# Kernel optimization log

Measured on AMD Instinct MI355X. Metric: run time of the kernel, lower is better.

Reference implementation:

```python
import jax, jax.numpy as jnp
import numpy as np

B, C, H, W = 64, 128, 32, 32
GROUPS = 32
EPS = 1e-6
SCALE = 0.044194173824159216  # 1/sqrt(512), as hardcoded in the torch module


def setup_inputs() -> dict:
    key = jax.random.key(0)
    ks = jax.random.split(key, 12)
    s = 1.0 / np.sqrt(C)
    return {
        "x": jax.random.normal(ks[0], (B, C, H, W), dtype=jnp.float32),
        "gn_w": jax.random.normal(ks[1], (C,), dtype=jnp.float32) * 0.02 + 1.0,
        "gn_b": jax.random.normal(ks[2], (C,), dtype=jnp.float32) * 0.02,
        "wq": jax.random.uniform(ks[3], (C, C), jnp.float32, -s, s),
        "bq": jax.random.uniform(ks[4], (C,), jnp.float32, -s, s),
        "wk": jax.random.uniform(ks[5], (C, C), jnp.float32, -s, s),
        "bk": jax.random.uniform(ks[6], (C,), jnp.float32, -s, s),
        "wv": jax.random.uniform(ks[7], (C, C), jnp.float32, -s, s),
        "bv": jax.random.uniform(ks[8], (C,), jnp.float32, -s, s),
        "wo": jax.random.uniform(ks[9], (C, C), jnp.float32, -s, s),
        "bo": jax.random.uniform(ks[10], (C,), jnp.float32, -s, s),
    }


def reference(x, gn_w, gn_b, wq, bq, wk, bk, wv, bv, wo, bo):
    b = x.shape[0]
    res = x
    # GroupNorm(32 groups, 128 channels): normalize over (channels_per_group, H, W)
    xg = x.reshape(b, GROUPS, C // GROUPS, H * W)
    mean = xg.mean(axis=(2, 3), keepdims=True)
    var = xg.var(axis=(2, 3), keepdims=True)
    xn = (xg - mean) * jax.lax.rsqrt(var + EPS)
    xn = xn.reshape(b, C, H, W) * gn_w[:, None, None] + gn_b[:, None, None]
    # flatten spatial -> sequence: [b, S=1024, C=128]
    t = xn.reshape(b, C, H * W).transpose(0, 2, 1)
    q = t @ wq.T + bq
    k = t @ wk.T + bk
    v = t @ wv.T + bv
    att = jnp.einsum('bsc,btc->bst', q, k) * SCALE  # [b, S, S]
    att = jax.nn.softmax(att, axis=-1)
    o = jnp.einsum('bst,btc->bsc', att, v)
    o = o @ wo.T + bo
    out = o.transpose(0, 2, 1).reshape(b, C, H, W) + res
    return out
```

## Files before the change

kernel.cpp:

```cpp
#include <hip/hip_runtime.h>
#include <hip/hip_bf16.h>

#define BATCH 64
#define CCH 128
#define SEQ 1024
#define NG 32
#define EPSV 1e-6f
#define SCALEV 0.044194173824159216f

typedef short v8s __attribute__((ext_vector_type(8)));
typedef short v4s __attribute__((ext_vector_type(4)));
typedef float v4f __attribute__((ext_vector_type(4)));
typedef int   v4i __attribute__((ext_vector_type(4)));
typedef unsigned short us;

__device__ __forceinline__ us f2bf(float f) {
    __hip_bfloat16 h = __float2bfloat16(f);
    return *reinterpret_cast<us*>(&h);
}

#define MFMA16(a, b, c) __builtin_amdgcn_mfma_f32_16x16x32_bf16(a, b, c, 0, 0, 0)

__device__ __forceinline__ void gld_lds16(const us* g, us* l) {
    __builtin_amdgcn_global_load_lds(
        (const __attribute__((address_space(1))) void*)g,
        (__attribute__((address_space(3))) void*)l, 16, 0, 0);
}

__global__ void prep_gn(const float* __restrict__ wq, const float* __restrict__ wk,
                        const float* __restrict__ wv, const float* __restrict__ wo,
                        us* wbf, const float* __restrict__ x,
                        float* meanr, float* rstdr) {
    int tid = threadIdx.x;
    if (blockIdx.x < 256) {
        int i = blockIdx.x * 256 + tid;
        const float* srcs[4] = {wq, wk, wv, wo};
        wbf[i] = f2bf(srcs[i >> 14][i & 16383]);
        return;
    }
    int bg = blockIdx.x - 256;
    const float4* p = (const float4*)(x + (size_t)bg * (4 * SEQ));
    float s1 = 0.f, s2 = 0.f;
    #pragma unroll
    for (int i = 0; i < 4; i++) {
        float4 v = p[i * 256 + tid];
        s1 += v.x + v.y + v.z + v.w;
        s2 += v.x * v.x + v.y * v.y + v.z * v.z + v.w * v.w;
    }
    #pragma unroll
    for (int off = 32; off; off >>= 1) {
        s1 += __shfl_down(s1, off);
        s2 += __shfl_down(s2, off);
    }
    __shared__ float a1[4], a2[4];
    int w = tid >> 6, l = tid & 63;
    if (l == 0) { a1[w] = s1; a2[w] = s2; }
    __syncthreads();
    if (tid == 0) {
        float t1 = a1[0] + a1[1] + a1[2] + a1[3];
        float t2 = a2[0] + a2[1] + a2[2] + a2[3];
        float mean = t1 * (1.0f / (4 * SEQ));
        float var  = t2 * (1.0f / (4 * SEQ)) - mean * mean;
        meanr[bg] = mean;
        rstdr[bg] = rsqrtf(var + EPSV);
    }
}

__global__ __launch_bounds__(256, 2) void qkv_kernel(
    const float* __restrict__ x, const float* __restrict__ gn_w,
    const float* __restrict__ gn_b, const float* __restrict__ meanr,
    const float* __restrict__ rstdr, const us* __restrict__ wbf,
    const float* __restrict__ bq, const float* __restrict__ bk,
    const float* __restrict__ bv,
    us* Q, us* K, us* Vt)
{
    __shared__ us tls[64 * 136];
    int b  = blockIdx.x >> 4;
    int s0 = (blockIdx.x & 15) * 64;
    int tid = threadIdx.x;
    const float* xb = x + (size_t)b * CCH * SEQ;

    for (int rep = 0; rep < 32; rep++) {
        int idx = rep * 256 + tid;
        int c = idx >> 6, s = idx & 63;
        float v = xb[c * SEQ + s0 + s];
        int g = c >> 2;
        float t = (v - meanr[b * NG + g]) * rstdr[b * NG + g] * gn_w[c] + gn_b[c];
        tls[s * 136 + c] = f2bf(t);
    }
    __syncthreads();

    int w = tid >> 6, lane = tid & 63;
    int m = lane & 15, quad = lane >> 4;

    v8s bfr[6][4];
    float bias[6];
    #pragma unroll
    for (int t = 0; t < 6; t++) {
        int T = w * 6 + t;
        int o = T >> 3, ct = T & 7;
        const us* wmat = wbf + o * 16384;
        #pragma unroll
        for (int ch = 0; ch < 4; ch++)
            bfr[t][ch] = *(const v8s*)&wmat[(ct * 16 + m) * 128 + ch * 32 + quad * 8];
        const float* bb = (o == 0) ? bq : (o == 1) ? bk : bv;
        bias[t] = bb[ct * 16 + m];
    }

    us* Qb = Q + (size_t)b * SEQ * CCH;
    us* Kb = K + (size_t)b * SEQ * CCH;
    us* Vb = Vt + (size_t)b * CCH * SEQ;

    #pragma unroll
    for (int st = 0; st < 4; st++) {
        v8s a[4];
        #pragma unroll
        for (int ch = 0; ch < 4; ch++)
            a[ch] = *(const v8s*)&tls[(st * 16 + m) * 136 + ch * 32 + quad * 8];
        int srow = s0 + st * 16 + quad * 4;
        #pragma unroll
        for (int t = 0; t < 6; t++) {
            int T = w * 6 + t;
            int o = T >> 3, ct = T & 7;
            v4f acc = {0,0,0,0};
            #pragma unroll
            for (int ch = 0; ch < 4; ch++)
                acc = MFMA16(a[ch], bfr[t][ch], acc);
            int col = ct * 16 + m;
            if (o < 2) {
                us* dst = (o == 0) ? Qb : Kb;
                #pragma unroll
                for (int r = 0; r < 4; r++)
                    dst[(size_t)(srow + r) * 128 + col] = f2bf(acc[r] + bias[t]);
            } else {
                v4s pk;
                #pragma unroll
                for (int r = 0; r < 4; r++) pk[r] = (short)f2bf(acc[r] + bias[t]);
                *(v4s*)&Vb[(size_t)col * SEQ + srow] = pk;
            }
        }
    }
}

__global__ __launch_bounds__(128, 2) void attn_kernel(
    const us* __restrict__ Q, const us* __restrict__ K,
    const us* __restrict__ Vt, const us* __restrict__ wbo,
    const float* __restrict__ bo, const float* __restrict__ x,
    float* __restrict__ out)
{
    __shared__ char smem_raw[32768];
    us* klds = (us*)smem_raw;
    us* vlds = (us*)(smem_raw + 16384);
    us* olds = (us*)smem_raw;

    int i = blockIdx.x;
    int b  = (i & 7) * 8 + ((i >> 3) & 7);
    int qt = i >> 6;
    int tid = threadIdx.x;
    int w = tid >> 6, lane = tid & 63;
    int m = lane & 15, quad = lane >> 4;
    int qrow0 = qt * 64 + w * 32;
    const us* Qb = Q + (size_t)b * SEQ * CCH;
    const us* Kb = K + (size_t)b * SEQ * CCH;
    const us* Vb = Vt + (size_t)b * CCH * SEQ;

    v8s aq[2][4];
    #pragma unroll
    for (int st = 0; st < 2; st++)
        #pragma unroll
        for (int ch = 0; ch < 4; ch++)
            aq[st][ch] = *(const v8s*)&Qb[(size_t)(qrow0 + st * 16 + m) * 128 + ch * 32 + quad * 8];

    v4f oacc[2][8];
    #pragma unroll
    for (int st = 0; st < 2; st++)
        #pragma unroll
        for (int ct = 0; ct < 8; ct++) oacc[st][ct] = (v4f){0, 0, 0, 0};
    float lrun[2] = {0.f, 0.f};

    const us* kg[8]; const us* vg[8];
    #pragma unroll
    for (int j8 = 0; j8 < 8; j8++) {
        int j = w * 8 + j8;
        int kr = 4 * j + (lane >> 4);
        kg[j8] = Kb + (size_t)kr * 128 + ((lane & 15) ^ (kr & 15)) * 8;
        int vc = 8 * j + (lane >> 3);
        vg[j8] = Vb + (size_t)vc * SEQ + ((lane & 7) ^ (vc & 7)) * 8;
    }
    int idx0 = 2 * (quad & 1) * 16 + m;
    int idx1 = idx0 + 16;

    for (int kt = 0; kt < 16; kt++) {
        __syncthreads();
        #pragma unroll
        for (int j8 = 0; j8 < 8; j8++) {
            int j = w * 8 + j8;
            gld_lds16(kg[j8] + kt * 8192, klds + j * 512);
            gld_lds16(vg[j8] + kt * 64,   vlds + j * 512);
        }
        __syncthreads();

        int e[2][4][2];
        #pragma unroll
        for (int c2 = 0; c2 < 4; c2++) {
            int krow = c2 * 16 + m;
            v4f acc0 = {0,0,0,0}, acc1 = {0,0,0,0};
            #pragma unroll
            for (int ch = 0; ch < 4; ch++) {
                int chunk = (ch * 4 + quad) ^ (krow & 15);
                v8s kb = *(const v8s*)&klds[krow * 128 + chunk * 8];
                acc0 = MFMA16(kb, aq[0][ch], acc0);
                acc1 = MFMA16(kb, aq[1][ch], acc1);
            }
            float p0[4], p1[4];
            #pragma unroll
            for (int r = 0; r < 4; r++) {
                p0[r] = __expf(acc0[r] * SCALEV);
                p1[r] = __expf(acc1[r] * SCALEV);
                lrun[0] += p0[r];
                lrun[1] += p1[r];
            }
            e[0][c2][0] = (int)f2bf(p0[0]) | ((int)f2bf(p0[1]) << 16);
            e[0][c2][1] = (int)f2bf(p0[2]) | ((int)f2bf(p0[3]) << 16);
            e[1][c2][0] = (int)f2bf(p1[0]) | ((int)f2bf(p1[1]) << 16);
            e[1][c2][1] = (int)f2bf(p1[2]) | ((int)f2bf(p1[3]) << 16);
        }
        v8s pa[2][2];
        #pragma unroll
        for (int st = 0; st < 2; st++)
            #pragma unroll
            for (int kc2 = 0; kc2 < 2; kc2++) {
                int c0 = (quad < 2) ? e[st][2 * kc2][0] : e[st][2 * kc2 + 1][0];
                int c1 = (quad < 2) ? e[st][2 * kc2][1] : e[st][2 * kc2 + 1][1];
                v4i t;
                t[0] = __shfl(c0, idx0);
                t[1] = __shfl(c1, idx0);
                t[2] = __shfl(c0, idx1);
                t[3] = __shfl(c1, idx1);
                pa[st][kc2] = __builtin_bit_cast(v8s, t);
            }
        #pragma unroll
        for (int ct = 0; ct < 8; ct++) {
            int vrow = ct * 16 + m;
            #pragma unroll
            for (int kc2 = 0; kc2 < 2; kc2++) {
                int chunk = (kc2 * 4 + quad) ^ (vrow & 7);
                v8s vb = *(const v8s*)&vlds[vrow * 64 + chunk * 8];
                oacc[0][ct] = MFMA16(pa[0][kc2], vb, oacc[0][ct]);
                oacc[1][ct] = MFMA16(pa[1][kc2], vb, oacc[1][ct]);
            }
        }
    }
    float inv[2][4];
    #pragma unroll
    for (int st = 0; st < 2; st++) {
        float rs = lrun[st];
        rs += __shfl_xor(rs, 16);
        rs += __shfl_xor(rs, 32);
        #pragma unroll
        for (int r = 0; r < 4; r++)
            inv[st][r] = 1.0f / __shfl(rs, quad * 4 + r);
    }
    __syncthreads();
    #pragma unroll
    for (int st = 0; st < 2; st++)
        #pragma unroll
        for (int ct = 0; ct < 8; ct++)
            #pragma unroll
            for (int r = 0; r < 4; r++)
                olds[(w * 32 + st * 16 + quad * 4 + r) * 136 + ct * 16 + m] =
                    f2bf(oacc[st][ct][r] * inv[st][r]);
    __syncthreads();
    const float* xb = x + (size_t)b * CCH * SEQ;
    float* ob = out + (size_t)b * CCH * SEQ;
    int sbase = qt * 64 + w * 32;
    v8s obf[2][4];
    #pragma unroll
    for (int st = 0; st < 2; st++)
        #pragma unroll
        for (int ch = 0; ch < 4; ch++)
            obf[st][ch] = *(const v8s*)&olds[(w * 32 + st * 16 + m) * 136 + ch * 32 + quad * 8];
    #pragma unroll
    for (int mt = 0; mt < 8; mt++) {
        v8s af[4];
        #pragma unroll
        for (int ch = 0; ch < 4; ch++)
            af[ch] = *(const v8s*)&wbo[(mt * 16 + m) * 128 + ch * 32 + quad * 8];
        #pragma unroll
        for (int st = 0; st < 2; st++) {
            v4f acc = {0,0,0,0};
            #pragma unroll
            for (int ch = 0; ch < 4; ch++)
                acc = MFMA16(af[ch], obf[st][ch], acc);
            #pragma unroll
            for (int r = 0; r < 4; r++) {
                int c = mt * 16 + quad * 4 + r;
                int idx = c * SEQ + sbase + st * 16 + m;
                ob[idx] = acc[r] + bo[c] + xb[idx];
            }
        }
    }
}

extern "C" void kernel_launch(void* const* d_in, const int* in_sizes, int n_in,
                              void* d_out, int out_size, void* d_ws, size_t ws_size,
                              hipStream_t stream) {
    const float* x    = (const float*)d_in[0];
    const float* gn_w = (const float*)d_in[1];
    const float* gn_b = (const float*)d_in[2];
    const float* wq   = (const float*)d_in[3];
    const float* bq   = (const float*)d_in[4];
    const float* wk   = (const float*)d_in[5];
    const float* bk   = (const float*)d_in[6];
    const float* wv   = (const float*)d_in[7];
    const float* bv   = (const float*)d_in[8];
    const float* wo   = (const float*)d_in[9];
    const float* bo   = (const float*)d_in[10];
    float* out = (float*)d_out;

    char* ws = (char*)d_ws;
    us* wbf      = (us*)ws;
    float* meanr = (float*)(ws + 131072);
    float* rstdr = (float*)(ws + 139264);
    us* Qbuf     = (us*)(ws + 147456);
    us* Kbuf     = (us*)(ws + 147456 + 16777216ull);
    us* Vtbuf    = (us*)(ws + 147456 + 2ull * 16777216ull);

    prep_gn<<<256 + BATCH * NG, 256, 0, stream>>>(wq, wk, wv, wo, wbf, x, meanr, rstdr);
    qkv_kernel<<<1024, 256, 0, stream>>>(x, gn_w, gn_b, meanr, rstdr, wbf,
                                         bq, bk, bv, Qbuf, Kbuf, Vtbuf);
    attn_kernel<<<1024, 128, 0, stream>>>(Qbuf, Kbuf, Vtbuf, wbf + 3 * 16384,
                                          bo, x, out);
}
```

Measured before the change: 180.4 us.

## Double-buffer K/V tiles in attention, use 4 waves of 16 rows, vectorize GN loads

```diff
diff --git a/kernel.cpp b/kernel.cpp
--- a/kernel.cpp
+++ b/kernel.cpp
@@ -75,18 +75,33 @@
     us* Q, us* K, us* Vt)
 {
     __shared__ us tls[64 * 136];
+    __shared__ float sa[CCH], sb[CCH];
     int b  = blockIdx.x >> 4;
     int s0 = (blockIdx.x & 15) * 64;
     int tid = threadIdx.x;
     const float* xb = x + (size_t)b * CCH * SEQ;
 
-    for (int rep = 0; rep < 32; rep++) {
+    if (tid < CCH) {
+        int g = tid >> 2;
+        float rs = rstdr[b * NG + g];
+        float mu = meanr[b * NG + g];
+        float a_ = rs * gn_w[tid];
+        sa[tid] = a_;
+        sb[tid] = gn_b[tid] - mu * a_;
+    }
+    __syncthreads();
+
+    #pragma unroll
+    for (int rep = 0; rep < 8; rep++) {
         int idx = rep * 256 + tid;
-        int c = idx >> 6, s = idx & 63;
-        float v = xb[c * SEQ + s0 + s];
-        int g = c >> 2;
-        float t = (v - meanr[b * NG + g]) * rstdr[b * NG + g] * gn_w[c] + gn_b[c];
-        tls[s * 136 + c] = f2bf(t);
+        int c = idx >> 4, s4 = idx & 15;
+        float4 v = *(const float4*)&xb[c * SEQ + s0 + s4 * 4];
+        float a_ = sa[c], b_ = sb[c];
+        int sbase = s4 * 4;
+        tls[(sbase + 0) * 136 + c] = f2bf(v.x * a_ + b_);
+        tls[(sbase + 1) * 136 + c] = f2bf(v.y * a_ + b_);
+        tls[(sbase + 2) * 136 + c] = f2bf(v.z * a_ + b_);
+        tls[(sbase + 3) * 136 + c] = f2bf(v.w * a_ + b_);
     }
     __syncthreads();
 
@@ -142,16 +157,13 @@
     }
 }
 
-__global__ __launch_bounds__(128, 2) void attn_kernel(
+__global__ __launch_bounds__(256, 2) void attn_kernel(
     const us* __restrict__ Q, const us* __restrict__ K,
     const us* __restrict__ Vt, const us* __restrict__ wbo,
     const float* __restrict__ bo, const float* __restrict__ x,
     float* __restrict__ out)
 {
-    __shared__ char smem_raw[32768];
-    us* klds = (us*)smem_raw;
-    us* vlds = (us*)(smem_raw + 16384);
-    us* olds = (us*)smem_raw;
+    __shared__ char smem_raw[65536];
 
     int i = blockIdx.x;
     int b  = (i & 7) * 8 + ((i >> 3) & 7);
@@ -159,145 +171,155 @@
     int tid = threadIdx.x;
     int w = tid >> 6, lane = tid & 63;
     int m = lane & 15, quad = lane >> 4;
-    int qrow0 = qt * 64 + w * 32;
+    int qrow0 = qt * 64 + w * 16;
     const us* Qb = Q + (size_t)b * SEQ * CCH;
     const us* Kb = K + (size_t)b * SEQ * CCH;
     const us* Vb = Vt + (size_t)b * CCH * SEQ;
 
-    v8s aq[2][4];
-    #pragma unroll
-    for (int st = 0; st < 2; st++)
-        #pragma unroll
-        for (int ch = 0; ch < 4; ch++)
-            aq[st][ch] = *(const v8s*)&Qb[(size_t)(qrow0 + st * 16 + m) * 128 + ch * 32 + quad * 8];
-
-    v4f oacc[2][8];
-    #pragma unroll
-    for (int st = 0; st < 2; st++)
-        #pragma unroll
-        for (int ct = 0; ct < 8; ct++) oacc[st][ct] = (v4f){0, 0, 0, 0};
-    float lrun[2] = {0.f, 0.f};
-
-    const us* kg[8]; const us* vg[8];
-    #pragma unroll
-    for (int j8 = 0; j8 < 8; j8++) {
-        int j = w * 8 + j8;
+    v8s aq[4];
+    #pragma unroll
+    for (int ch = 0; ch < 4; ch++)
+        aq[ch] = *(const v8s*)&Qb[(size_t)(qrow0 + m) * 128 + ch * 32 + quad * 8];
+
+    v4f oacc[8];
+    #pragma unroll
+    for (int ct = 0; ct < 8; ct++) oacc[ct] = (v4f){0, 0, 0, 0};
+    float lrun = 0.f;
+
+    const us* kg[4]; const us* vg[4];
+    int jb = w * 4;
+    #pragma unroll
+    for (int j4 = 0; j4 < 4; j4++) {
+        int j = jb + j4;
         int kr = 4 * j + (lane >> 4);
-        kg[j8] = Kb + (size_t)kr * 128 + ((lane & 15) ^ (kr & 15)) * 8;
+        kg[j4] = Kb + (size_t)kr * 128 + ((lane & 15) ^ (kr & 15)) * 8;
         int vc = 8 * j + (lane >> 3);
-        vg[j8] = Vb + (size_t)vc * SEQ + ((lane & 7) ^ (vc & 7)) * 8;
+        vg[j4] = Vb + (size_t)vc * SEQ + ((lane & 7) ^ (vc & 7)) * 8;
     }
     int idx0 = 2 * (quad & 1) * 16 + m;
     int idx1 = idx0 + 16;
 
+    #pragma unroll
+    for (int j4 = 0; j4 < 4; j4++) {
+        gld_lds16(kg[j4], (us*)smem_raw + (jb + j4) * 512);
+        gld_lds16(vg[j4], (us*)(smem_raw + 16384) + (jb + j4) * 512);
+    }
+
     for (int kt = 0; kt < 16; kt++) {
-        __syncthreads();
-        #pragma unroll
-        for (int j8 = 0; j8 < 8; j8++) {
-            int j = w * 8 + j8;
-            gld_lds16(kg[j8] + kt * 8192, klds + j * 512);
-            gld_lds16(vg[j8] + kt * 64,   vlds + j * 512);
-        }
-        __syncthreads();
-
-        int e[2][4][2];
+        int boff  = (kt & 1) ? 32768 : 0;
+        int boffn = boff ^ 32768;
+        __builtin_amdgcn_s_barrier();
+        if (kt < 15) {
+            #pragma unroll
+            for (int j4 = 0; j4 < 4; j4++) {
+                gld_lds16(kg[j4] + (size_t)(kt + 1) * 8192,
+                          (us*)(smem_raw + boffn) + (jb + j4) * 512);
+                gld_lds16(vg[j4] + (size_t)(kt + 1) * 64,
+                          (us*)(smem_raw + boffn + 16384) + (jb + j4) * 512);
+            }
+            asm volatile("s_waitcnt vmcnt(8)" ::: "memory");
+        } else {
+            asm volatile("s_waitcnt vmcnt(0)" ::: "memory");
+        }
+        __builtin_amdgcn_s_barrier();
+
+        const us* kl = (const us*)(smem_raw + boff);
+        const us* vl = (const us*)(smem_raw + boff + 16384);
+
+        v4f acc[4];
+        __builtin_amdgcn_s_setprio(1);
         #pragma unroll
         for (int c2 = 0; c2 < 4; c2++) {
             int krow = c2 * 16 + m;
-            v4f acc0 = {0,0,0,0}, acc1 = {0,0,0,0};
+            acc[c2] = (v4f){0, 0, 0, 0};
             #pragma unroll
             for (int ch = 0; ch < 4; ch++) {
                 int chunk = (ch * 4 + quad) ^ (krow & 15);
-                v8s kb = *(const v8s*)&klds[krow * 128 + chunk * 8];
-                acc0 = MFMA16(kb, aq[0][ch], acc0);
-                acc1 = MFMA16(kb, aq[1][ch], acc1);
-            }
-            float p0[4], p1[4];
+                v8s kb = *(const v8s*)&kl[krow * 128 + chunk * 8];
+                acc[c2] = MFMA16(kb, aq[ch], acc[c2]);
+            }
+        }
+        __builtin_amdgcn_s_setprio(0);
+
+        int e[4][2];
+        #pragma unroll
+        for (int c2 = 0; c2 < 4; c2++) {
+            float p[4];
             #pragma unroll
             for (int r = 0; r < 4; r++) {
-                p0[r] = __expf(acc0[r] * SCALEV);
-                p1[r] = __expf(acc1[r] * SCALEV);
-                lrun[0] += p0[r];
-                lrun[1] += p1[r];
-            }
-            e[0][c2][0] = (int)f2bf(p0[0]) | ((int)f2bf(p0[1]) << 16);
-            e[0][c2][1] = (int)f2bf(p0[2]) | ((int)f2bf(p0[3]) << 16);
-            e[1][c2][0] = (int)f2bf(p1[0]) | ((int)f2bf(p1[1]) << 16);
-            e[1][c2][1] = (int)f2bf(p1[2]) | ((int)f2bf(p1[3]) << 16);
-        }
-        v8s pa[2][2];
-        #pragma unroll
-        for (int st = 0; st < 2; st++)
-            #pragma unroll
-            for (int kc2 = 0; kc2 < 2; kc2++) {
-                int c0 = (quad < 2) ? e[st][2 * kc2][0] : e[st][2 * kc2 + 1][0];
-                int c1 = (quad < 2) ? e[st][2 * kc2][1] : e[st][2 * kc2 + 1][1];
-                v4i t;
-                t[0] = __shfl(c0, idx0);
-                t[1] = __shfl(c1, idx0);
-                t[2] = __shfl(c0, idx1);
-                t[3] = __shfl(c1, idx1);
-                pa[st][kc2] = __builtin_bit_cast(v8s, t);
-            }
+                p[r] = __expf(acc[c2][r] * SCALEV);
+                lrun += p[r];
+            }
+            e[c2][0] = (int)f2bf(p[0]) | ((int)f2bf(p[1]) << 16);
+            e[c2][1] = (int)f2bf(p[2]) | ((int)f2bf(p[3]) << 16);
+        }
+        v8s pa[2];
+        #pragma unroll
+        for (int kc2 = 0; kc2 < 2; kc2++) {
+            int c0 = (quad < 2) ? e[2 * kc2][0] : e[2 * kc2 + 1][0];
+            int c1 = (quad < 2) ? e[2 * kc2][1] : e[2 * kc2 + 1][1];
+            v4i t;
+            t[0] = __shfl(c0, idx0);
+            t[1] = __shfl(c1, idx0);
+            t[2] = __shfl(c0, idx1);
+            t[3] = __shfl(c1, idx1);
+            pa[kc2] = __builtin_bit_cast(v8s, t);
+        }
+        __builtin_amdgcn_s_setprio(1);
         #pragma unroll
         for (int ct = 0; ct < 8; ct++) {
             int vrow = ct * 16 + m;
             #pragma unroll
             for (int kc2 = 0; kc2 < 2; kc2++) {
                 int chunk = (kc2 * 4 + quad) ^ (vrow & 7);
-                v8s vb = *(const v8s*)&vlds[vrow * 64 + chunk * 8];
-                oacc[0][ct] = MFMA16(pa[0][kc2], vb, oacc[0][ct]);
-                oacc[1][ct] = MFMA16(pa[1][kc2], vb, oacc[1][ct]);
-            }
-        }
-    }
-    float inv[2][4];
-    #pragma unroll
-    for (int st = 0; st < 2; st++) {
-        float rs = lrun[st];
+                v8s vb = *(const v8s*)&vl[vrow * 64 + chunk * 8];
+                oacc[ct] = MFMA16(pa[kc2], vb, oacc[ct]);
+            }
+        }
+        __builtin_amdgcn_s_setprio(0);
+    }
+
+    float inv[4];
+    {
+        float rs = lrun;
         rs += __shfl_xor(rs, 16);
         rs += __shfl_xor(rs, 32);
         #pragma unroll
         for (int r = 0; r < 4; r++)
-            inv[st][r] = 1.0f / __shfl(rs, quad * 4 + r);
-    }
-    __syncthreads();
-    #pragma unroll
-    for (int st = 0; st < 2; st++)
-        #pragma unroll
-        for (int ct = 0; ct < 8; ct++)
-            #pragma unroll
-            for (int r = 0; r < 4; r++)
-                olds[(w * 32 + st * 16 + quad * 4 + r) * 136 + ct * 16 + m] =
-                    f2bf(oacc[st][ct][r] * inv[st][r]);
-    __syncthreads();
+            inv[r] = 1.0f / __shfl(rs, quad * 4 + r);
+    }
+    __syncthreads();
+    us* olds = (us*)smem_raw;
+    #pragma unroll
+    for (int ct = 0; ct < 8; ct++)
+        #pragma unroll
+        for (int r = 0; r < 4; r++)
+            olds[(w * 16 + quad * 4 + r) * 136 + ct * 16 + m] =
+                f2bf(oacc[ct][r] * inv[r]);
+    __syncthreads();
+
     const float* xb = x + (size_t)b * CCH * SEQ;
     float* ob = out + (size_t)b * CCH * SEQ;
-    int sbase = qt * 64 + w * 32;
-    v8s obf[2][4];
-    #pragma unroll
-    for (int st = 0; st < 2; st++)
-        #pragma unroll
-        for (int ch = 0; ch < 4; ch++)
-            obf[st][ch] = *(const v8s*)&olds[(w * 32 + st * 16 + m) * 136 + ch * 32 + quad * 8];
+    int sbase = qt * 64 + w * 16;
+    v8s obf[4];
+    #pragma unroll
+    for (int ch = 0; ch < 4; ch++)
+        obf[ch] = *(const v8s*)&olds[(w * 16 + m) * 136 + ch * 32 + quad * 8];
     #pragma unroll
     for (int mt = 0; mt < 8; mt++) {
         v8s af[4];
         #pragma unroll
         for (int ch = 0; ch < 4; ch++)
             af[ch] = *(const v8s*)&wbo[(mt * 16 + m) * 128 + ch * 32 + quad * 8];
-        #pragma unroll
-        for (int st = 0; st < 2; st++) {
-            v4f acc = {0,0,0,0};
-            #pragma unroll
-            for (int ch = 0; ch < 4; ch++)
-                acc = MFMA16(af[ch], obf[st][ch], acc);
-            #pragma unroll
-            for (int r = 0; r < 4; r++) {
-                int c = mt * 16 + quad * 4 + r;
-                int idx = c * SEQ + sbase + st * 16 + m;
-                ob[idx] = acc[r] + bo[c] + xb[idx];
-            }
+        v4f acc = {0,0,0,0};
+        #pragma unroll
+        for (int ch = 0; ch < 4; ch++)
+            acc = MFMA16(af[ch], obf[ch], acc);
+        #pragma unroll
+        for (int r = 0; r < 4; r++) {
+            int c = mt * 16 + quad * 4 + r;
+            int idx = c * SEQ + sbase + m;
+            ob[idx] = acc[r] + bo[c] + xb[idx];
         }
     }
 }
@@ -329,6 +351,6 @@
     prep_gn<<<256 + BATCH * NG, 256, 0, stream>>>(wq, wk, wv, wo, wbf, x, meanr, rstdr);
     qkv_kernel<<<1024, 256, 0, stream>>>(x, gn_w, gn_b, meanr, rstdr, wbf,
                                          bq, bk, bv, Qbuf, Kbuf, Vtbuf);
-    attn_kernel<<<1024, 128, 0, stream>>>(Qbuf, Kbuf, Vtbuf, wbf + 3 * 16384,
+    attn_kernel<<<1024, 256, 0, stream>>>(Qbuf, Kbuf, Vtbuf, wbf + 3 * 16384,
                                           bo, x, out);
 }
```

Result: slower. 187.6 us (+3.9%).
